# Kernel optimization log

Hardware: AMD Instinct MI355X
Metric: run time of the kernel (lower is better)

## Reference

```python
import jax, jax.numpy as jnp
import numpy as np

BS, NPTS, NM, D = 8, 8192, 32, 512  # objects, points/object, masks/object, feature dim


def setup_inputs() -> dict:
    key = jax.random.key(0)
    k1, k2, k3 = jax.random.split(key, 3)
    net_out = jax.random.normal(k1, (BS * NPTS, D), dtype=jnp.float32)
    mask_embs = jax.random.normal(k2, (BS * NM, D), dtype=jnp.float32)
    mask_pts = (jax.random.uniform(k3, (BS, NM, NPTS)) < 0.5).astype(jnp.float32)
    pt_offset = (jnp.arange(1, BS + 1) * NPTS).astype(jnp.int32)  # per-object end idx
    logit_scale = jnp.float32(2.6593)  # ln(1/0.07), CLIP-style
    return {
        "net_out": net_out,
        "mask_embs": mask_embs,
        "mask_pts": mask_pts,
        "logit_scale": logit_scale,
        "pt_offset": pt_offset,
    }


def reference(net_out, mask_embs, mask_pts, logit_scale, pt_offset):
    bs, nm, npts = mask_pts.shape
    d = net_out.shape[1]
    n_total = bs * nm

    # ragged per-object mask_pt @ net_out[start:end] -> uniform batched matmul
    net = net_out.reshape(bs, npts, d)
    sum_feats = jnp.einsum('bmp,bpd->bmd', mask_pts, net).reshape(n_total, d)

    mask_npts = jnp.sum(mask_pts, axis=-1).reshape(n_total, 1)  # points per mask
    nopts = (mask_npts[:, 0] == 0)                              # empty masks -> ignored
    avg_feats = sum_feats / (mask_npts + 1e-12)

    logits = (mask_embs @ avg_feats.T) * jnp.exp(logit_scale)   # [N, N]

    idx = jnp.arange(n_total)
    valid = ~nopts  # target == -100 (ignore) for empty masks, else arange diagonal
    texts_loss = jnp.where(valid, -jax.nn.log_softmax(logits, axis=-1)[idx, idx], 0.0)
    pts_loss = jnp.where(valid, -jax.nn.log_softmax(logits.T, axis=-1)[idx, idx], 0.0)

    def nonzero_avg(l):
        cnt = jnp.sum(l > 0)
        return jnp.where(cnt > 0, jnp.sum(l) / jnp.maximum(cnt, 1), 0.0)

    return (nonzero_avg(texts_loss) + nonzero_avg(pts_loss)) / 2.0
```

## Files before the change

### kernel.cpp

```cpp
#include <hip/hip_runtime.h>
#include <hip/hip_bf16.h>
#include <math.h>

#define BS 8
#define NPTS 8192
#define NM 32
#define D 512
#define NT (BS*NM)
#define KC 32
#define KCHUNK (NPTS/KC)
#define TILES (KCHUNK/32)
#define DC 8
#define DCHUNK (D/DC)
#define NWORDS (NPTS/32)

#define LOG2E 1.44269504088896f
#define LN2   0.69314718055995f

typedef short short8 __attribute__((ext_vector_type(8)));
typedef float f32x4 __attribute__((ext_vector_type(4)));

static constexpr size_t OFF_SUMF = 0;
static constexpr size_t OFF_CNTS = OFF_SUMF + (size_t)NT*D;
static constexpr size_t OFF_BITS = OFF_CNTS + NT;
static constexpr size_t OFF_LOG  = OFF_BITS + (size_t)NT*NWORDS;
static constexpr size_t OFF_RLSE = OFF_LOG + (size_t)NT*NT;
static constexpr size_t OFF_CLSE = OFF_RLSE + NT;
static constexpr size_t OFF_TICK = OFF_CLSE + NT;

__device__ __forceinline__ short bf16_rne(float f) {
  return __builtin_bit_cast(short, __float2bfloat16(f));
}

__global__ __launch_bounds__(256) void kp_prep(const float* __restrict__ mpts,
                                               unsigned int* __restrict__ mbits,
                                               float* __restrict__ cnts,
                                               float* __restrict__ sumf,
                                               int* __restrict__ ticket) {
  const int n = blockIdx.x;
  const int t = threadIdx.x;
  if (n == 0 && t == 0) *ticket = 0;
  const float4* mp = (const float4*)(mpts + ((size_t)n << 13) + t * 32);
  unsigned int u = 0;
  #pragma unroll
  for (int q = 0; q < 8; ++q) {
    const float4 v = mp[q];
    u |= (v.x != 0.f ? 1u : 0u) << (q * 4 + 0);
    u |= (v.y != 0.f ? 1u : 0u) << (q * 4 + 1);
    u |= (v.z != 0.f ? 1u : 0u) << (q * 4 + 2);
    u |= (v.w != 0.f ? 1u : 0u) << (q * 4 + 3);
  }
  mbits[n * NWORDS + t] = u;
  ((float2*)(sumf + ((size_t)n << 9)))[t] = make_float2(0.f, 0.f);
  int c = __popc(u);
  #pragma unroll
  for (int o = 32; o > 0; o >>= 1) c += __shfl_down(c, o, 64);
  __shared__ int red[4];
  if ((t & 63) == 0) red[t >> 6] = c;
  __syncthreads();
  if (t == 0) cnts[n] = (float)(red[0] + red[1] + red[2] + red[3]);
}

__global__ __launch_bounds__(256, 8) void k1_mfma(const float* __restrict__ net,
                                                  const unsigned int* __restrict__ mbits,
                                                  float* __restrict__ sumf) {
  const int bx = blockIdx.x;
  const int dc = bx & 7;
  const int kc = (bx >> 3) & 31;
  const int b  = bx >> 8;
  const int w    = threadIdx.x >> 6;
  const int lane = threadIdx.x & 63;
  const int lhi = lane >> 4, llo = lane & 15;
  const int k0 = kc * KCHUNK;
  const int d0 = dc * DCHUNK + w * 16;

  const unsigned int* r0 = mbits + (size_t)(b * NM + llo) * NWORDS + kc * TILES;
  const unsigned int* r1 = r0 + (size_t)16 * NWORDS;

  const float* np_ = net + (((size_t)(b * NPTS + k0 + lhi * 8)) << 9) + d0 + llo;

  f32x4 acc0 = {0.f, 0.f, 0.f, 0.f};
  f32x4 acc1 = {0.f, 0.f, 0.f, 0.f};
  const int sh = lhi * 8;

  #pragma unroll 4
  for (int t = 0; t < TILES; ++t) {
    const unsigned int u0 = r0[t];
    const unsigned int u1 = r1[t];

    float bv[8];
    #pragma unroll
    for (int j = 0; j < 8; ++j) bv[j] = np_[(size_t)j << 9];

    short8 bf, a0f, a1f;
    #pragma unroll
    for (int j = 0; j < 8; ++j) bf[j] = bf16_rne(bv[j]);
    const unsigned int b0 = (u0 >> sh) & 0xffu;
    const unsigned int b1 = (u1 >> sh) & 0xffu;
    #pragma unroll
    for (int j = 0; j < 8; ++j) {
      a0f[j] = (short)(-(int)((b0 >> j) & 1u) & 0x3F80);
      a1f[j] = (short)(-(int)((b1 >> j) & 1u) & 0x3F80);
    }

    acc0 = __builtin_amdgcn_mfma_f32_16x16x32_bf16(a0f, bf, acc0, 0, 0, 0);
    acc1 = __builtin_amdgcn_mfma_f32_16x16x32_bf16(a1f, bf, acc1, 0, 0, 0);

    np_ += (size_t)32 << 9;
  }

  float* sp = sumf + (((size_t)(b * NM)) << 9) + d0 + llo;
  #pragma unroll
  for (int j = 0; j < 4; ++j) {
    atomicAdd(sp + ((size_t)(lhi * 4 + j) << 9),      acc0[j]);
    atomicAdd(sp + ((size_t)(16 + lhi * 4 + j) << 9), acc1[j]);
  }
}

__global__ __launch_bounds__(128) void k2_logits(const float* __restrict__ embs,
                                                 const float* __restrict__ sumf,
                                                 const float* __restrict__ cnts,
                                                 const float* __restrict__ lsc,
                                                 float* __restrict__ logits) {
  const int h = threadIdx.x >> 6;
  const int lane = threadIdx.x & 63;
  const int wt = blockIdx.x;
  const int ti = wt >> 4, tj = wt & 15;
  const int lhi = lane >> 4, llo = lane & 15;

  const float* ea = embs + (((size_t)(ti * 16 + llo)) << 9) + h * 256 + lhi * 8;
  const float* sv = sumf + (((size_t)(tj * 16 + llo)) << 9) + h * 256 + lhi * 8;
  f32x4 acc = {0.f, 0.f, 0.f, 0.f};
  #pragma unroll
  for (int kk = 0; kk < 8; ++kk) {
    const float4 e0 = *(const float4*)(ea);
    const float4 e1 = *(const float4*)(ea + 4);
    const float4 v0 = *(const float4*)(sv);
    const float4 v1 = *(const float4*)(sv + 4);
    const float ev[8] = {e0.x, e0.y, e0.z, e0.w, e1.x, e1.y, e1.z, e1.w};
    const float vv[8] = {v0.x, v0.y, v0.z, v0.w, v1.x, v1.y, v1.z, v1.w};
    short8 ef, vf;
    #pragma unroll
    for (int j = 0; j < 8; ++j) { ef[j] = bf16_rne(ev[j]); vf[j] = bf16_rne(vv[j]); }
    acc = __builtin_amdgcn_mfma_f32_16x16x32_bf16(ef, vf, acc, 0, 0, 0);
    ea += 32; sv += 32;
  }

  __shared__ float part[64 * 4];
  if (h == 1) *(float4*)(&part[lane * 4]) = make_float4(acc[0], acc[1], acc[2], acc[3]);
  __syncthreads();
  if (h == 0) {
    const float4 p = *(const float4*)(&part[lane * 4]);
    const float scale = expf(lsc[0]);
    const float invc = scale / (cnts[tj * 16 + llo] + 1e-12f);
    float* lp = logits + (size_t)(ti * 16) * NT + tj * 16 + llo;
    lp[(size_t)(lhi * 4 + 0) * NT] = (acc[0] + p.x) * invc;
    lp[(size_t)(lhi * 4 + 1) * NT] = (acc[1] + p.y) * invc;
    lp[(size_t)(lhi * 4 + 2) * NT] = (acc[2] + p.z) * invc;
    lp[(size_t)(lhi * 4 + 3) * NT] = (acc[3] + p.w) * invc;
  }
}

__global__ __launch_bounds__(256) void k3_lse(const float* __restrict__ logits,
                                              float* __restrict__ rowlse,
                                              float* __restrict__ clse,
                                              const float* __restrict__ cnts,
                                              int* __restrict__ ticket,
                                              float* __restrict__ out) {
  const int g = blockIdx.x;
  const int r = threadIdx.x >> 4;
  const int c = threadIdx.x & 15;
  __shared__ float red[16][17];
  if (g < 16) {
    const int col = g * 16 + c;
    float mx = -1e30f;
    #pragma unroll 4
    for (int kk = 0; kk < 16; ++kk)
      mx = fmaxf(mx, logits[(size_t)(kk * 16 + r) * NT + col]);
    red[r][c] = mx; __syncthreads();
    for (int st = 8; st; st >>= 1) { if (r < st) red[r][c] = fmaxf(red[r][c], red[r + st][c]); __syncthreads(); }
    const float mx2 = red[0][c] * LOG2E; __syncthreads();
    float s = 0.f;
    #pragma unroll 4
    for (int kk = 0; kk < 16; ++kk)
      s += exp2f(logits[(size_t)(kk * 16 + r) * NT + col] * LOG2E - mx2);
    red[r][c] = s; __syncthreads();
    for (int st = 8; st; st >>= 1) { if (r < st) red[r][c] += red[r + st][c]; __syncthreads(); }
    if (r == 0) clse[col] = (mx2 + log2f(red[0][c])) * LN2;
  } else {
    const int row = (g - 16) * 16 + r;
    float mx = -1e30f;
    #pragma unroll 4
    for (int kk = 0; kk < 16; ++kk)
      mx = fmaxf(mx, logits[(size_t)row * NT + kk * 16 + c]);
    #pragma unroll
    for (int o = 8; o; o >>= 1) mx = fmaxf(mx, __shfl_xor(mx, o, 64));
    const float mx2 = mx * LOG2E;
    float s = 0.f;
    #pragma unroll 4
    for (int kk = 0; kk < 16; ++kk)
      s += exp2f(logits[(size_t)row * NT + kk * 16 + c] * LOG2E - mx2);
    #pragma unroll
    for (int o = 8; o; o >>= 1) s += __shfl_xor(s, o, 64);
    if (c == 0) rowlse[row] = (mx2 + log2f(s)) * LN2;
  }

  __shared__ int slast;
  __syncthreads();
  if (threadIdx.x == 0) {
    __threadfence();
    slast = (atomicAdd(ticket, 1) == 31);
  }
  __syncthreads();
  if (!slast) return;
  __threadfence();

  const int i = threadIdx.x;
  const float diag = logits[(size_t)i * NT + i];
  const bool valid = cnts[i] > 0.f;
  const float tl = valid ? (rowlse[i] - diag) : 0.f;
  const float pl = valid ? (clse[i] - diag) : 0.f;

  __shared__ float fred[4][256];
  fred[0][i] = tl;
  fred[1][i] = (tl > 0.f) ? 1.f : 0.f;
  fred[2][i] = pl;
  fred[3][i] = (pl > 0.f) ? 1.f : 0.f;
  __syncthreads();
  for (int st = 128; st > 0; st >>= 1) {
    if (i < st) {
      fred[0][i] += fred[0][i + st];
      fred[1][i] += fred[1][i + st];
      fred[2][i] += fred[2][i + st];
      fred[3][i] += fred[3][i + st];
    }
    __syncthreads();
  }
  if (i == 0) {
    const float a1 = (fred[1][0] > 0.f) ? fred[0][0] / fmaxf(fred[1][0], 1.f) : 0.f;
    const float a2 = (fred[3][0] > 0.f) ? fred[2][0] / fmaxf(fred[3][0], 1.f) : 0.f;
    out[0] = 0.5f * (a1 + a2);
  }
}

extern "C" void kernel_launch(void* const* d_in, const int* in_sizes, int n_in,
                              void* d_out, int out_size, void* d_ws, size_t ws_size,
                              hipStream_t stream) {
  const float* net  = (const float*)d_in[0];
  const float* embs = (const float*)d_in[1];
  const float* mpts = (const float*)d_in[2];
  const float* lsc  = (const float*)d_in[3];

  float* ws     = (float*)d_ws;
  float* sumf   = ws + OFF_SUMF;
  float* cnts   = ws + OFF_CNTS;
  unsigned int* mbits = (unsigned int*)(ws + OFF_BITS);
  float* logits = ws + OFF_LOG;
  float* rowlse = ws + OFF_RLSE;
  float* clse   = ws + OFF_CLSE;
  int*   ticket = (int*)(ws + OFF_TICK);
  float* outp   = (float*)d_out;

  kp_prep<<<dim3(NT), dim3(256), 0, stream>>>(mpts, mbits, cnts, sumf, ticket);
  k1_mfma<<<dim3(BS * KC * DC), dim3(256), 0, stream>>>(net, mbits, sumf);
  k2_logits<<<dim3(NT), dim3(128), 0, stream>>>(embs, sumf, cnts, lsc, logits);
  k3_lse<<<dim3(32), dim3(256), 0, stream>>>(logits, rowlse, clse, cnts, ticket, outp);
}
```

Before: 50.66 us.

## Widen k1 per-wave D tile to 64 columns with float4 loads

Each wave of the masked-sum MFMA kernel now covers 64 feature columns instead of 16. It loads net_out rows with float4 and issues four MFMAs per mask-half per tile, reusing the same A fragments. The grid shrinks fourfold (DC 8 to 2) and launch bounds drop to 2 blocks per CU. This cuts redundant mask-fragment construction and gives wider, coalesced global loads, in exchange for more registers, fewer blocks to hide latency, and a permuted column mapping that the atomic store must undo.

Result: slower. 95.28 us (+88.1%).

```diff
diff --git a/kernel.cpp b/kernel.cpp
--- a/kernel.cpp
+++ b/kernel.cpp
@@ -10,8 +10,7 @@
 #define KC 32
 #define KCHUNK (NPTS/KC)
 #define TILES (KCHUNK/32)
-#define DC 8
-#define DCHUNK (D/DC)
+#define DC 2
 #define NWORDS (NPTS/32)
 
 #define LOG2E 1.44269504088896f
@@ -61,40 +60,44 @@
   if (t == 0) cnts[n] = (float)(red[0] + red[1] + red[2] + red[3]);
 }
 
-__global__ __launch_bounds__(256, 8) void k1_mfma(const float* __restrict__ net,
+__global__ __launch_bounds__(256, 2) void k1_mfma(const float* __restrict__ net,
                                                   const unsigned int* __restrict__ mbits,
                                                   float* __restrict__ sumf) {
   const int bx = blockIdx.x;
-  const int dc = bx & 7;
-  const int kc = (bx >> 3) & 31;
-  const int b  = bx >> 8;
+  const int dc = bx & 1;
+  const int kc = (bx >> 1) & 31;
+  const int b  = bx >> 6;
   const int w    = threadIdx.x >> 6;
   const int lane = threadIdx.x & 63;
   const int lhi = lane >> 4, llo = lane & 15;
   const int k0 = kc * KCHUNK;
-  const int d0 = dc * DCHUNK + w * 16;
+  const int d0 = dc * 256 + w * 64;
 
   const unsigned int* r0 = mbits + (size_t)(b * NM + llo) * NWORDS + kc * TILES;
   const unsigned int* r1 = r0 + (size_t)16 * NWORDS;
 
-  const float* np_ = net + (((size_t)(b * NPTS + k0 + lhi * 8)) << 9) + d0 + llo;
-
-  f32x4 acc0 = {0.f, 0.f, 0.f, 0.f};
-  f32x4 acc1 = {0.f, 0.f, 0.f, 0.f};
+  const float* np_ = net + (((size_t)(b * NPTS + k0 + lhi * 8)) << 9) + d0 + llo * 4;
+
+  f32x4 acc0[4] = {{0.f,0.f,0.f,0.f},{0.f,0.f,0.f,0.f},{0.f,0.f,0.f,0.f},{0.f,0.f,0.f,0.f}};
+  f32x4 acc1[4] = {{0.f,0.f,0.f,0.f},{0.f,0.f,0.f,0.f},{0.f,0.f,0.f,0.f},{0.f,0.f,0.f,0.f}};
   const int sh = lhi * 8;
 
-  #pragma unroll 4
+  #pragma unroll 2
   for (int t = 0; t < TILES; ++t) {
     const unsigned int u0 = r0[t];
     const unsigned int u1 = r1[t];
 
-    float bv[8];
-    #pragma unroll
-    for (int j = 0; j < 8; ++j) bv[j] = np_[(size_t)j << 9];
-
-    short8 bf, a0f, a1f;
-    #pragma unroll
-    for (int j = 0; j < 8; ++j) bf[j] = bf16_rne(bv[j]);
+    short8 bfc0, bfc1, bfc2, bfc3;
+    #pragma unroll
+    for (int j = 0; j < 8; ++j) {
+      const float4 v = *(const float4*)(np_ + ((size_t)j << 9));
+      bfc0[j] = bf16_rne(v.x);
+      bfc1[j] = bf16_rne(v.y);
+      bfc2[j] = bf16_rne(v.z);
+      bfc3[j] = bf16_rne(v.w);
+    }
+
+    short8 a0f, a1f;
     const unsigned int b0 = (u0 >> sh) & 0xffu;
     const unsigned int b1 = (u1 >> sh) & 0xffu;
     #pragma unroll
@@ -103,17 +106,26 @@
       a1f[j] = (short)(-(int)((b1 >> j) & 1u) & 0x3F80);
     }
 
-    acc0 = __builtin_amdgcn_mfma_f32_16x16x32_bf16(a0f, bf, acc0, 0, 0, 0);
-    acc1 = __builtin_amdgcn_mfma_f32_16x16x32_bf16(a1f, bf, acc1, 0, 0, 0);
+    acc0[0] = __builtin_amdgcn_mfma_f32_16x16x32_bf16(a0f, bfc0, acc0[0], 0, 0, 0);
+    acc0[1] = __builtin_amdgcn_mfma_f32_16x16x32_bf16(a0f, bfc1, acc0[1], 0, 0, 0);
+    acc0[2] = __builtin_amdgcn_mfma_f32_16x16x32_bf16(a0f, bfc2, acc0[2], 0, 0, 0);
+    acc0[3] = __builtin_amdgcn_mfma_f32_16x16x32_bf16(a0f, bfc3, acc0[3], 0, 0, 0);
+    acc1[0] = __builtin_amdgcn_mfma_f32_16x16x32_bf16(a1f, bfc0, acc1[0], 0, 0, 0);
+    acc1[1] = __builtin_amdgcn_mfma_f32_16x16x32_bf16(a1f, bfc1, acc1[1], 0, 0, 0);
+    acc1[2] = __builtin_amdgcn_mfma_f32_16x16x32_bf16(a1f, bfc2, acc1[2], 0, 0, 0);
+    acc1[3] = __builtin_amdgcn_mfma_f32_16x16x32_bf16(a1f, bfc3, acc1[3], 0, 0, 0);
 
     np_ += (size_t)32 << 9;
   }
 
-  float* sp = sumf + (((size_t)(b * NM)) << 9) + d0 + llo;
-  #pragma unroll
-  for (int j = 0; j < 4; ++j) {
-    atomicAdd(sp + ((size_t)(lhi * 4 + j) << 9),      acc0[j]);
-    atomicAdd(sp + ((size_t)(16 + lhi * 4 + j) << 9), acc1[j]);
+  float* spb = sumf + (((size_t)(b * NM)) << 9) + d0 + llo * 4;
+  #pragma unroll
+  for (int c = 0; c < 4; ++c) {
+    #pragma unroll
+    for (int j = 0; j < 4; ++j) {
+      atomicAdd(spb + ((size_t)(lhi * 4 + j) << 9) + c,      acc0[c][j]);
+      atomicAdd(spb + ((size_t)(16 + lhi * 4 + j) << 9) + c, acc1[c][j]);
+    }
   }
 }
 
```
